# Optimization experiments

Measured on AMD Instinct MI355X. Metric: run time of the kernel, lower is better.

Reference implementation:

```python
import jax, jax.numpy as jnp
import numpy as np
from jax import lax

B, C, H, W, S = 2, 64, 32, 32, 16
KS = 5  # conv2 kernel size


def setup_inputs() -> dict:
    key = jax.random.key(0)
    k0, k1, k2 = jax.random.split(key, 3)
    x = jax.random.normal(k0, (B, C, H, W, S), jnp.float32)
    # conv1: 1x1 Conv2d(C -> 3C)
    w1 = jax.random.normal(k1, (3 * C, C, 1, 1), jnp.float32) / np.sqrt(C)
    b1 = jnp.zeros((3 * C,), jnp.float32)
    # conv2: Conv2d(2C -> 1, KSxKS, reflect 'same')
    w2 = jax.random.normal(k2, (1, 2 * C, KS, KS), jnp.float32) / np.sqrt(2 * C * KS * KS)
    b2 = jnp.zeros((1,), jnp.float32)
    return {"x": x, "w1": w1, "b1": b1, "w2": w2, "b2": b2}


def _conv_same_reflect(z, w):
    # z: [N, Cin, H, W], w: [Cout, Cin, k, k]; 'same' with reflect padding
    p = w.shape[-1] // 2
    zp = jnp.pad(z, ((0, 0), (0, 0), (p, p), (p, p)), mode="reflect")
    return lax.conv_general_dilated(zp, w, (1, 1), "VALID",
                                    dimension_numbers=("NCHW", "OIHW", "NCHW"))


def reference(x, w1, b1, w2, b2):
    b, c, h, w, s = x.shape
    # conv1 (1x1) applied per frame == channel mixing einsum
    qkv = jnp.einsum("oc,bchws->bohws", w1[:, :, 0, 0], x) + b1[None, :, None, None, None]
    Q, K, V = jnp.split(qkv, 3, axis=1)  # each [b,c,h,w,s]

    # conv2 on concat(Q[...,s], K[...,t]) is linear in channels:
    # score = conv(Q_s; w2[:, :c]) + conv(K_t; w2[:, c:]) + bias
    def half_score(z, wpart):
        zf = jnp.transpose(z, (0, 4, 1, 2, 3)).reshape(b * s, c, h, w)
        sc = _conv_same_reflect(zf, wpart)[:, 0]  # (b*s, h, w)
        return sc.reshape(b, s, h, w)

    sQ = half_score(Q, w2[:, :c])  # [b, s(query), h, w]
    sK = half_score(K, w2[:, c:])  # [b, t(key),   h, w]

    # score[b,h,w,t,s]
    score = (jnp.transpose(sQ, (0, 2, 3, 1))[:, :, :, None, :]
             + jnp.transpose(sK, (0, 2, 3, 1))[:, :, :, :, None]
             + b2[0])
    attn = jax.nn.softmax(score, axis=-2)  # softmax over key index t
    # V_out[b,c,h,w,s] = sum_t attn[b,h,w,t,s] * V[b,c,h,w,t]
    return jnp.einsum("bhwts,bchwt->bchws", attn, V)
```

## Files before the change

### kernel.cpp

```cpp
#include <hip/hip_runtime.h>


__device__ __forceinline__ int reflect32(int i) {
    if (i < 0) i = -i;
    if (i >= 32) i = 62 - i;
    return i;
}

__global__ void k_fuse(const float* __restrict__ w1, const float* __restrict__ w2,
                       float* __restrict__ Akp) {
    int k  = blockIdx.x;
    int cp = threadIdx.x;
    float acc = 0.f;
    if (k < 25) {
        for (int c = 0; c < 64; ++c)
            acc += w2[(64 + c) * 25 + k] * w1[(64 + c) * 64 + cp];
    }
    Akp[cp * 28 + k] = acc;
}

__global__ void __launch_bounds__(64) k_gemm(const float* __restrict__ x,
                                             const float* __restrict__ Akp,
                                             float* __restrict__ u) {
    __shared__ float4 aks[64 * 7];
    int tid = threadIdx.x;
    const float4* Ak4 = (const float4*)Akp;
    for (int j = tid; j < 448; j += 64) aks[j] = Ak4[j];
    __syncthreads();

    int idx = blockIdx.x * 64 + tid;
    int b   = idx >> 14;
    int pt  = idx & 16383;
    const float* xp = x + b * 1048576 + pt;

    float acc[28];
#pragma unroll
    for (int k = 0; k < 28; ++k) acc[k] = 0.f;

    for (int c = 0; c < 64; ++c) {
        float xv = xp[c * 16384];
#pragma unroll
        for (int q = 0; q < 7; ++q) {
            float4 a = aks[c * 7 + q];
            acc[q * 4 + 0] = fmaf(a.x, xv, acc[q * 4 + 0]);
            acc[q * 4 + 1] = fmaf(a.y, xv, acc[q * 4 + 1]);
            acc[q * 4 + 2] = fmaf(a.z, xv, acc[q * 4 + 2]);
            acc[q * 4 + 3] = fmaf(a.w, xv, acc[q * 4 + 3]);
        }
    }
#pragma unroll
    for (int k = 0; k < 25; ++k) u[k * 32768 + idx] = acc[k];
}

__global__ void __launch_bounds__(256) k_attn(const float* __restrict__ x,
                                              const float* __restrict__ u,
                                              const float* __restrict__ w1,
                                              const float* __restrict__ b1,
                                              float* __restrict__ out) {
    __shared__ float wT[64 * 65];
    __shared__ float sk_s[4 * 16];
    __shared__ float y_s[4 * 64];

    int tid = threadIdx.x;
    int g0  = blockIdx.x * 4;
    int b   = g0 >> 10;
    int p0  = g0 & 1023;

    for (int j = tid; j < 4096; j += 256)
        wT[(j & 63) * 65 + (j >> 6)] = w1[8192 + j];

    if (tid < 64) {
        int pix = tid >> 4, t = tid & 15;
        int p = p0 + pix;
        int h = p >> 5, w = p & 31;
        float acc = 0.f;
#pragma unroll
        for (int ky = 0; ky < 5; ++ky) {
            int rh = reflect32(h + ky - 2);
#pragma unroll
            for (int kx = 0; kx < 5; ++kx) {
                int rw = reflect32(w + kx - 2);
                int k  = ky * 5 + kx;
                acc += u[k * 32768 + b * 16384 + (rh * 32 + rw) * 16 + t];
            }
        }
        sk_s[pix * 16 + t] = acc;
    }
    __syncthreads();

    int cc = tid & 63, pix = tid >> 6;
    int p  = p0 + pix;
    float sk[16];
#pragma unroll
    for (int t = 0; t < 16; ++t) sk[t] = sk_s[pix * 16 + t];
    float m = sk[0];
#pragma unroll
    for (int t = 1; t < 16; ++t) m = fmaxf(m, sk[t]);
    float e[16];
    float ssum = 0.f;
#pragma unroll
    for (int t = 0; t < 16; ++t) { e[t] = __expf(sk[t] - m); ssum += e[t]; }
    float inv = 1.0f / ssum;

    const float4* xp = (const float4*)(x + b * 1048576 + cc * 16384 + p * 16);
    float y = 0.f;
#pragma unroll
    for (int q = 0; q < 4; ++q) {
        float4 xv = xp[q];
        y += e[4 * q + 0] * xv.x + e[4 * q + 1] * xv.y +
             e[4 * q + 2] * xv.z + e[4 * q + 3] * xv.w;
    }
    y_s[pix * 64 + cc] = y * inv;
    __syncthreads();

    float acc = b1[128 + cc];
#pragma unroll 8
    for (int i = 0; i < 64; ++i)
        acc = fmaf(wT[i * 65 + cc], y_s[pix * 64 + i], acc);

    float4 v = make_float4(acc, acc, acc, acc);
    float4* op = (float4*)(out + (size_t)(b * 64 + cc) * 16384 + p * 16);
    op[0] = v; op[1] = v; op[2] = v; op[3] = v;
}

extern "C" void kernel_launch(void* const* d_in, const int* in_sizes, int n_in,
                              void* d_out, int out_size, void* d_ws, size_t ws_size,
                              hipStream_t stream) {
    const float* x  = (const float*)d_in[0];
    const float* w1 = (const float*)d_in[1];
    const float* b1 = (const float*)d_in[2];
    const float* w2 = (const float*)d_in[3];
    float* out = (float*)d_out;
    float* ws  = (float*)d_ws;

    float* Akp = ws;
    float* u   = ws + 2048;

    k_fuse<<<28, 64, 0, stream>>>(w1, w2, Akp);
    k_gemm<<<512, 64, 0, stream>>>(x, Akp, u);
    k_attn<<<512, 256, 0, stream>>>(x, u, w1, b1, out);
}
```

Measured before the change: 89.12 us.

## Split gemm outputs across two waves and restructure attention kernel work distribution

k_gemm now runs two waves per block, each computing about half of the 25 conv taps. Weights are read through scalar (wave-uniform) loads instead of a shared-memory staging copy. k_attn stages the x tile into shared memory with coalesced float4 loads and spreads the 25-tap reflect gather across all 256 threads, where before only 64 threads did it. The final channel-mixing matvec is reorganised so each thread does four pixels over a quarter of the inputs, with shuffle reductions, and writes contiguous float4 stores. The aim is more parallelism and better coalescing, at the cost of some redundant x reads in gemm and extra synchronisation in attn.

```diff
diff --git a/kernel.cpp b/kernel.cpp
--- a/kernel.cpp
+++ b/kernel.cpp
@@ -19,37 +19,36 @@
     Akp[cp * 28 + k] = acc;
 }
 
-__global__ void __launch_bounds__(64) k_gemm(const float* __restrict__ x,
-                                             const float* __restrict__ Akp,
-                                             float* __restrict__ u) {
-    __shared__ float4 aks[64 * 7];
-    int tid = threadIdx.x;
-    const float4* Ak4 = (const float4*)Akp;
-    for (int j = tid; j < 448; j += 64) aks[j] = Ak4[j];
-    __syncthreads();
-
-    int idx = blockIdx.x * 64 + tid;
-    int b   = idx >> 14;
-    int pt  = idx & 16383;
+__global__ void __launch_bounds__(128) k_gemm(const float* __restrict__ x,
+                                              const float* __restrict__ Akp,
+                                              float* __restrict__ u) {
+    int tid  = threadIdx.x;
+    int wave = tid >> 6;
+    int l    = tid & 63;
+    int idx  = blockIdx.x * 64 + l;
+    int b    = idx >> 14;
+    int pt   = idx & 16383;
     const float* xp = x + b * 1048576 + pt;
 
-    float acc[28];
+    int k0 = __builtin_amdgcn_readfirstlane(wave ? 12 : 0);
+
+    float acc[13];
 #pragma unroll
-    for (int k = 0; k < 28; ++k) acc[k] = 0.f;
+    for (int k = 0; k < 13; ++k) acc[k] = 0.f;
 
+#pragma unroll 4
     for (int c = 0; c < 64; ++c) {
         float xv = xp[c * 16384];
+        const float* ak = Akp + c * 28 + k0;
 #pragma unroll
-        for (int q = 0; q < 7; ++q) {
-            float4 a = aks[c * 7 + q];
-            acc[q * 4 + 0] = fmaf(a.x, xv, acc[q * 4 + 0]);
-            acc[q * 4 + 1] = fmaf(a.y, xv, acc[q * 4 + 1]);
-            acc[q * 4 + 2] = fmaf(a.z, xv, acc[q * 4 + 2]);
-            acc[q * 4 + 3] = fmaf(a.w, xv, acc[q * 4 + 3]);
-        }
+        for (int k = 0; k < 13; ++k)
+            acc[k] = fmaf(ak[k], xv, acc[k]);
     }
+
+    int kstart = wave ? 1 : 0;
 #pragma unroll
-    for (int k = 0; k < 25; ++k) u[k * 32768 + idx] = acc[k];
+    for (int k = 0; k < 13; ++k)
+        if (k >= kstart) u[(k0 + k) * 32768 + idx] = acc[k];
 }
 
 __global__ void __launch_bounds__(256) k_attn(const float* __restrict__ x,
@@ -58,69 +57,100 @@
                                               const float* __restrict__ b1,
                                               float* __restrict__ out) {
     __shared__ float wT[64 * 65];
-    __shared__ float sk_s[4 * 16];
-    __shared__ float y_s[4 * 64];
+    __shared__ float xs[4 * 1040];
+    __shared__ float psk[4 * 64];
+    __shared__ float sk_s[64];
+    __shared__ float ysT[64 * 4];
 
     int tid = threadIdx.x;
     int g0  = blockIdx.x * 4;
     int b   = g0 >> 10;
     int p0  = g0 & 1023;
 
-    for (int j = tid; j < 4096; j += 256)
-        wT[(j & 63) * 65 + (j >> 6)] = w1[8192 + j];
+    {
+        int cc = tid >> 2, sub = tid & 3;
+        const float* xbase = x + b * 1048576 + cc * 16384 + p0 * 16 + sub * 4;
+#pragma unroll
+        for (int pix = 0; pix < 4; ++pix) {
+            float4 v = *(const float4*)(xbase + pix * 16);
+            float* dst = xs + pix * 1040 + (4 * sub) * 65 + cc;
+            dst[0] = v.x; dst[65] = v.y; dst[130] = v.z; dst[195] = v.w;
+        }
+    }
+    for (int e = tid; e < 4096; e += 256)
+        wT[(e & 63) * 65 + (e >> 6)] = w1[8192 + e];
 
-    if (tid < 64) {
-        int pix = tid >> 4, t = tid & 15;
-        int p = p0 + pix;
-        int h = p >> 5, w = p & 31;
+    {
+        int grp = tid >> 6;
+        int pix = (tid >> 4) & 3;
+        int t   = tid & 15;
+        int p   = p0 + pix;
+        int hh  = p >> 5, ww = p & 31;
+        int kk0 = grp * 7;
+        int nk  = (grp == 3) ? 4 : 7;
+        const float* ub = u + b * 16384 + t;
         float acc = 0.f;
+        for (int q = 0; q < nk; ++q) {
+            int k  = kk0 + q;
+            int ky = k / 5, kx = k - ky * 5;
+            int rh = reflect32(hh + ky - 2);
+            int rw = reflect32(ww + kx - 2);
+            acc += ub[k * 32768 + (rh * 32 + rw) * 16];
+        }
+        psk[grp * 64 + pix * 16 + t] = acc;
+    }
+    __syncthreads();
+    if (tid < 64)
+        sk_s[tid] = psk[tid] + psk[64 + tid] + psk[128 + tid] + psk[192 + tid];
+    __syncthreads();
+
+    {
+        int pix = tid >> 6, cc = tid & 63;
+        float sk[16];
 #pragma unroll
-        for (int ky = 0; ky < 5; ++ky) {
-            int rh = reflect32(h + ky - 2);
+        for (int t = 0; t < 16; ++t) sk[t] = sk_s[pix * 16 + t];
+        float m = sk[0];
 #pragma unroll
-            for (int kx = 0; kx < 5; ++kx) {
-                int rw = reflect32(w + kx - 2);
-                int k  = ky * 5 + kx;
-                acc += u[k * 32768 + b * 16384 + (rh * 32 + rw) * 16 + t];
-            }
-        }
-        sk_s[pix * 16 + t] = acc;
+        for (int t = 1; t < 16; ++t) m = fmaxf(m, sk[t]);
+        float e[16], ssum = 0.f;
+#pragma unroll
+        for (int t = 0; t < 16; ++t) { e[t] = __expf(sk[t] - m); ssum += e[t]; }
+        float inv = 1.0f / ssum;
+
+        const float* xr = xs + pix * 1040 + cc;
+        float y = 0.f;
+#pragma unroll
+        for (int t = 0; t < 16; ++t) y = fmaf(e[t], xr[t * 65], y);
+        ysT[cc * 4 + pix] = y * inv;
     }
     __syncthreads();
 
-    int cc = tid & 63, pix = tid >> 6;
-    int p  = p0 + pix;
-    float sk[16];
+    {
+        int cc = tid >> 2, sub = tid & 3;
+        float o0 = 0.f, o1 = 0.f, o2 = 0.f, o3 = 0.f;
 #pragma unroll
-    for (int t = 0; t < 16; ++t) sk[t] = sk_s[pix * 16 + t];
-    float m = sk[0];
-#pragma unroll
-    for (int t = 1; t < 16; ++t) m = fmaxf(m, sk[t]);
-    float e[16];
-    float ssum = 0.f;
-#pragma unroll
-    for (int t = 0; t < 16; ++t) { e[t] = __expf(sk[t] - m); ssum += e[t]; }
-    float inv = 1.0f / ssum;
+        for (int ii = 0; ii < 16; ++ii) {
+            int i = ii * 4 + sub;
+            float wv = wT[i * 65 + cc];
+            float4 yv = *(const float4*)(ysT + i * 4);
+            o0 = fmaf(wv, yv.x, o0);
+            o1 = fmaf(wv, yv.y, o1);
+            o2 = fmaf(wv, yv.z, o2);
+            o3 = fmaf(wv, yv.w, o3);
+        }
+        o0 += __shfl_xor(o0, 1); o0 += __shfl_xor(o0, 2);
+        o1 += __shfl_xor(o1, 1); o1 += __shfl_xor(o1, 2);
+        o2 += __shfl_xor(o2, 1); o2 += __shfl_xor(o2, 2);
+        o3 += __shfl_xor(o3, 1); o3 += __shfl_xor(o3, 2);
+        float bb = b1[128 + cc];
+        o0 += bb; o1 += bb; o2 += bb; o3 += bb;
 
-    const float4* xp = (const float4*)(x + b * 1048576 + cc * 16384 + p * 16);
-    float y = 0.f;
-#pragma unroll
-    for (int q = 0; q < 4; ++q) {
-        float4 xv = xp[q];
-        y += e[4 * q + 0] * xv.x + e[4 * q + 1] * xv.y +
-             e[4 * q + 2] * xv.z + e[4 * q + 3] * xv.w;
+        float* ob = out + (size_t)(b * 64 + cc) * 16384 + p0 * 16 + sub * 4;
+        *(float4*)(ob +  0) = make_float4(o0, o0, o0, o0);
+        *(float4*)(ob + 16) = make_float4(o1, o1, o1, o1);
+        *(float4*)(ob + 32) = make_float4(o2, o2, o2, o2);
+        *(float4*)(ob + 48) = make_float4(o3, o3, o3, o3);
     }
-    y_s[pix * 64 + cc] = y * inv;
-    __syncthreads();
-
-    float acc = b1[128 + cc];
-#pragma unroll 8
-    for (int i = 0; i < 64; ++i)
-        acc = fmaf(wT[i * 65 + cc], y_s[pix * 64 + i], acc);
-
-    float4 v = make_float4(acc, acc, acc, acc);
-    float4* op = (float4*)(out + (size_t)(b * 64 + cc) * 16384 + p * 16);
-    op[0] = v; op[1] = v; op[2] = v; op[3] = v;
 }
 
 extern "C" void kernel_launch(void* const* d_in, const int* in_sizes, int n_in,
@@ -137,6 +167,6 @@
     float* u   = ws + 2048;
 
     k_fuse<<<28, 64, 0, stream>>>(w1, w2, Akp);
-    k_gemm<<<512, 64, 0, stream>>>(x, Akp, u);
+    k_gemm<<<512, 128, 0, stream>>>(x, Akp, u);
     k_attn<<<512, 256, 0, stream>>>(x, u, w1, b1, out);
 }
```

New measurement: 88.49 us. No clear change (-0.7%).
